# Kernel optimization log

Measured on AMD Instinct MI355X. Metric: run time of the kernel, lower is better.

## Reference

```python
import jax, jax.numpy as jnp
import numpy as np

P = 1024 * 1024  # pixels (coordinate rows) the CPPN is evaluated on
N_IN, H, N_OUT = 12, 32, 3

# Activation library (CPPN-style): 0=identity, 1=tanh, 2=sigmoid, 3=sin, 4=gaussian
_ACTS = [
    lambda x: x,
    jnp.tanh,
    jax.nn.sigmoid,
    jnp.sin,
    lambda x: jnp.exp(-0.5 * x * x),
]

def _apply_acts(pre, ids):
    # pre: [P, n], ids: [n] int per-node activation id (Node.set_activation)
    out = pre
    for k, f in enumerate(_ACTS):
        if k == 0:
            out = f(pre)
        else:
            out = jnp.where(ids == k, f(pre), out)
    return out


def setup_inputs() -> dict:
    key = jax.random.key(0)
    ks = jax.random.split(key, 12)
    def w(k, shape, fan_in):
        return jax.random.normal(k, shape, jnp.float32) / np.sqrt(fan_in)
    inputs = jax.random.normal(ks[0], (P, N_IN), jnp.float32)
    return {
        "inputs": inputs,
        "bias_in": jnp.zeros((N_IN,), jnp.float32),
        "W1": w(ks[1], (N_IN, H), N_IN),
        "b1": 0.1 * jax.random.normal(ks[2], (H,), jnp.float32),
        "act1": jax.random.randint(ks[3], (H,), 0, 5, jnp.int32),
        "W2": w(ks[4], (H, H), H),
        "b2": 0.1 * jax.random.normal(ks[5], (H,), jnp.float32),
        "act2": jax.random.randint(ks[6], (H,), 0, 5, jnp.int32),
        "W3": w(ks[7], (H, H), H),
        "b3": 0.1 * jax.random.normal(ks[8], (H,), jnp.float32),
        "act3": jax.random.randint(ks[9], (H,), 0, 5, jnp.int32),
        "Wout": w(ks[10], (H, N_OUT), H),
        "bout": 0.1 * jax.random.normal(ks[11], (N_OUT,), jnp.float32),
    }


def reference(inputs, bias_in, W1, b1, act1, W2, b2, act2, W3, b3, act3, Wout, bout):
    # Input nodes: Node.forward = identity(x + bias)
    h0 = inputs + bias_in
    # Each hidden layer: per-edge scalar multiply + sum (== matvec since fully
    # connected between consecutive layers), then per-node bias + activation.
    h1 = _apply_acts(h0 @ W1 + b1, act1)
    h2 = _apply_acts(h1 @ W2 + b2, act2)
    h3 = _apply_acts(h2 @ W3 + b3, act3)
    # Output nodes use config.output_activation = tanh
    return jnp.tanh(h3 @ Wout + bout)
```

## Files before the change

kernel.cpp:

```cpp
#include <hip/hip_runtime.h>
#include <hip/hip_bf16.h>


#define BLK 256
#define NT 16

constexpr int NIN = 12, HID = 32, NOUT = 3;

typedef __attribute__((ext_vector_type(8))) short short8v;
typedef __attribute__((ext_vector_type(4))) float f32x4;

__device__ __forceinline__ unsigned short f2bf(float f) {
    unsigned u = __builtin_bit_cast(unsigned, f);
    u += 0x7FFFu + ((u >> 16) & 1u);
    return (unsigned short)(u >> 16);
}

__device__ __forceinline__ float tanh_fast(float x) {
    float e = __expf(2.0f * x);
    return 1.0f - 2.0f * __builtin_amdgcn_rcpf(e + 1.0f);
}

__device__ __forceinline__ float act_apply(float x, int id) {
    float e_in = (id == 1) ? (x + x) : ((id == 4) ? (-0.5f * x * x) : -x);
    float e = __expf(e_in);
    float r = __builtin_amdgcn_rcpf(e + 1.0f);
    float res = x;
    res = (id == 1) ? fmaf(-2.0f, r, 1.0f) : res;
    res = (id == 2) ? r : res;
    res = (id == 3) ? __sinf(x) : res;
    res = (id == 4) ? e : res;
    return res;
}

__global__ void __launch_bounds__(BLK, 4) cppn_mfma(
    const float* __restrict__ xin, const float* __restrict__ bin,
    const float* __restrict__ W1, const float* __restrict__ b1, const int* __restrict__ a1,
    const float* __restrict__ W2, const float* __restrict__ b2, const int* __restrict__ a2,
    const float* __restrict__ W3, const float* __restrict__ b3, const int* __restrict__ a3,
    const float* __restrict__ Wo, const float* __restrict__ bo,
    float* __restrict__ out, int Ppix) {
    const int tid = threadIdx.x;
    const int lane = tid & 63;
    const int wid = tid >> 6;
    const int q = lane >> 4;
    const int l15 = lane & 15;

    short8v w1f[2], w2f[2], w3f[2], wof;
#pragma unroll
    for (int t = 0; t < 2; ++t) {
#pragma unroll
        for (int j = 0; j < 8; ++j) {
            int k1 = 8 * q + j;
            float v1 = (k1 < NIN) ? W1[k1 * HID + 16 * t + l15]
                     : (k1 == NIN ? b1[16 * t + l15] : 0.0f);
            w1f[t][j] = (short)f2bf(v1);
            int k2 = 16 * (j >> 2) + 4 * q + (j & 3);
            w2f[t][j] = (short)f2bf(W2[k2 * HID + 16 * t + l15]);
            w3f[t][j] = (short)f2bf(W3[k2 * HID + 16 * t + l15]);
        }
    }
#pragma unroll
    for (int j = 0; j < 8; ++j) {
        int k2 = 16 * (j >> 2) + 4 * q + (j & 3);
        wof[j] = (l15 < NOUT) ? (short)f2bf(Wo[k2 * NOUT + l15]) : (short)0;
    }

    f32x4 b2f[2], b3f[2], bof;
#pragma unroll
    for (int t = 0; t < 2; ++t) {
#pragma unroll
        for (int r = 0; r < 4; ++r) {
            b2f[t][r] = b2[16 * t + 4 * q + r];
            b3f[t][r] = b3[16 * t + 4 * q + r];
        }
    }
#pragma unroll
    for (int r = 0; r < 4; ++r) bof[r] = (q == 0 && r < NOUT) ? bo[r] : 0.0f;

    int a1v[8], a2v[8], a3v[8];
#pragma unroll
    for (int e = 0; e < 8; ++e) {
        int j = 16 * (e >> 2) + 4 * q + (e & 3);
        a1v[e] = a1[j]; a2v[e] = a2[j]; a3v[e] = a3[j];
    }

    float binv[8];
#pragma unroll
    for (int j = 0; j < 8; ++j) {
        int k = 8 * q + j;
        binv[j] = (k < NIN) ? bin[k] : 0.0f;
    }

    const long long waveIdx = (long long)blockIdx.x * (BLK / 64) + wid;
    const long long px0 = waveIdx * (NT * 16);
    const f32x4 z = {0.0f, 0.0f, 0.0f, 0.0f};

    for (int it = 0; it < NT; ++it) {
        const long long px = px0 + it * 16 + l15;
        const bool ok = (px < Ppix);

        short8v b0f = {0, 0, 0, 0, 0, 0, 0, 0};
        if (q == 0) {
            f32x4 xa = ok ? *reinterpret_cast<const f32x4*>(xin + px * NIN)     : z;
            f32x4 xb = ok ? *reinterpret_cast<const f32x4*>(xin + px * NIN + 4) : z;
#pragma unroll
            for (int j = 0; j < 4; ++j) b0f[j]     = (short)f2bf(xa[j] + binv[j]);
#pragma unroll
            for (int j = 0; j < 4; ++j) b0f[4 + j] = (short)f2bf(xb[j] + binv[4 + j]);
        } else if (q == 1) {
            f32x4 xc = ok ? *reinterpret_cast<const f32x4*>(xin + px * NIN + 8) : z;
#pragma unroll
            for (int j = 0; j < 4; ++j) b0f[j] = (short)f2bf(xc[j] + binv[j]);
            b0f[4] = (short)0x3F80;
        }

        f32x4 p0 = __builtin_amdgcn_mfma_f32_16x16x32_bf16(w1f[0], b0f, z, 0, 0, 0);
        f32x4 p1 = __builtin_amdgcn_mfma_f32_16x16x32_bf16(w1f[1], b0f, z, 0, 0, 0);
        short8v hb;
#pragma unroll
        for (int r = 0; r < 4; ++r) hb[r]     = (short)f2bf(act_apply(p0[r], a1v[r]));
#pragma unroll
        for (int r = 0; r < 4; ++r) hb[4 + r] = (short)f2bf(act_apply(p1[r], a1v[4 + r]));

        p0 = __builtin_amdgcn_mfma_f32_16x16x32_bf16(w2f[0], hb, b2f[0], 0, 0, 0);
        p1 = __builtin_amdgcn_mfma_f32_16x16x32_bf16(w2f[1], hb, b2f[1], 0, 0, 0);
#pragma unroll
        for (int r = 0; r < 4; ++r) hb[r]     = (short)f2bf(act_apply(p0[r], a2v[r]));
#pragma unroll
        for (int r = 0; r < 4; ++r) hb[4 + r] = (short)f2bf(act_apply(p1[r], a2v[4 + r]));

        p0 = __builtin_amdgcn_mfma_f32_16x16x32_bf16(w3f[0], hb, b3f[0], 0, 0, 0);
        p1 = __builtin_amdgcn_mfma_f32_16x16x32_bf16(w3f[1], hb, b3f[1], 0, 0, 0);
#pragma unroll
        for (int r = 0; r < 4; ++r) hb[r]     = (short)f2bf(act_apply(p0[r], a3v[r]));
#pragma unroll
        for (int r = 0; r < 4; ++r) hb[4 + r] = (short)f2bf(act_apply(p1[r], a3v[4 + r]));

        f32x4 o = __builtin_amdgcn_mfma_f32_16x16x32_bf16(wof, hb, bof, 0, 0, 0);
        if (q == 0 && ok) {
            out[px * 3 + 0] = tanh_fast(o[0]);
            out[px * 3 + 1] = tanh_fast(o[1]);
            out[px * 3 + 2] = tanh_fast(o[2]);
        }
    }
}

extern "C" void kernel_launch(void* const* d_in, const int* in_sizes, int n_in,
                              void* d_out, int out_size, void* d_ws, size_t ws_size,
                              hipStream_t stream) {
    (void)n_in; (void)out_size; (void)d_ws; (void)ws_size;
    const float* xin = (const float*)d_in[0];
    const float* bin = (const float*)d_in[1];
    const float* W1  = (const float*)d_in[2];
    const float* b1  = (const float*)d_in[3];
    const int*   a1  = (const int*)  d_in[4];
    const float* W2  = (const float*)d_in[5];
    const float* b2  = (const float*)d_in[6];
    const int*   a2  = (const int*)  d_in[7];
    const float* W3  = (const float*)d_in[8];
    const float* b3  = (const float*)d_in[9];
    const int*   a3  = (const int*)  d_in[10];
    const float* Wo  = (const float*)d_in[11];
    const float* bo  = (const float*)d_in[12];
    float* out = (float*)d_out;

    const int Ppix = in_sizes[0] / NIN;
    const int pxPerBlock = (BLK / 64) * NT * 16;
    const int grid = (Ppix + pxPerBlock - 1) / pxPerBlock;
    hipLaunchKernelGGL(cppn_mfma, dim3(grid), dim3(BLK), 0, stream,
                       xin, bin, W1, b1, a1, W2, b2, a2, W3, b3, a3, Wo, bo,
                       out, Ppix);
}
```

Baseline: 202.2 us.

## Use packed bf16 conversion, bit-packed activation ids, exp2 chain and unguarded main kernel

Replaces the manual bf16 rounding with the v_cvt_pk_bf16_f32 instruction, which converts two floats at once. The per-node activation ids are packed into one 32-bit register per layer, so 24 registers of ids are no longer held. The activation evaluation is rewritten around exp2f with a prescaled input, and the pixel loop is kept rolled. A template GUARD parameter splits the launch into a full-block kernel with no bounds checks and a separate tail kernel, which adds a second launch when the pixel count is not a multiple of the block size.

```diff
diff --git a/kernel.cpp b/kernel.cpp
--- a/kernel.cpp
+++ b/kernel.cpp
@@ -9,6 +9,7 @@
 
 typedef __attribute__((ext_vector_type(8))) short short8v;
 typedef __attribute__((ext_vector_type(4))) float f32x4;
+typedef __attribute__((ext_vector_type(4))) unsigned uint4v;
 
 __device__ __forceinline__ unsigned short f2bf(float f) {
     unsigned u = __builtin_bit_cast(unsigned, f);
@@ -16,30 +17,42 @@
     return (unsigned short)(u >> 16);
 }
 
+__device__ __forceinline__ unsigned cvt_pk(float lo, float hi) {
+    unsigned r;
+    asm("v_cvt_pk_bf16_f32 %0, %1, %2" : "=v"(r) : "v"(lo), "v"(hi));
+    return r;
+}
+
 __device__ __forceinline__ float tanh_fast(float x) {
     float e = __expf(2.0f * x);
     return 1.0f - 2.0f * __builtin_amdgcn_rcpf(e + 1.0f);
 }
 
-__device__ __forceinline__ float act_apply(float x, int id) {
-    float e_in = (id == 1) ? (x + x) : ((id == 4) ? (-0.5f * x * x) : -x);
-    float e = __expf(e_in);
+__device__ __forceinline__ float act_chain(float x, int sid) {
+    const float L = 1.4426950408889634f;
+    const bool is1 = (sid == 1), is2 = (sid == 2), is3 = (sid == 3), is4 = (sid == 4);
+    float u = x * L;
+    float ein = is1 ? (u + u) : -u;
+    float g = (u * -0.5f) * x;
+    ein = is4 ? g : ein;
+    float e = exp2f(ein);
     float r = __builtin_amdgcn_rcpf(e + 1.0f);
-    float res = x;
-    res = (id == 1) ? fmaf(-2.0f, r, 1.0f) : res;
-    res = (id == 2) ? r : res;
-    res = (id == 3) ? __sinf(x) : res;
-    res = (id == 4) ? e : res;
-    return res;
-}
-
+    float y = is1 ? fmaf(-2.0f, r, 1.0f) : x;
+    y = is2 ? r : y;
+    y = is4 ? e : y;
+    float s = __sinf(x);
+    y = is3 ? s : y;
+    return y;
+}
+
+template <bool GUARD>
 __global__ void __launch_bounds__(BLK, 4) cppn_mfma(
     const float* __restrict__ xin, const float* __restrict__ bin,
     const float* __restrict__ W1, const float* __restrict__ b1, const int* __restrict__ a1,
     const float* __restrict__ W2, const float* __restrict__ b2, const int* __restrict__ a2,
     const float* __restrict__ W3, const float* __restrict__ b3, const int* __restrict__ a3,
     const float* __restrict__ Wo, const float* __restrict__ bo,
-    float* __restrict__ out, int Ppix) {
+    float* __restrict__ out, int Ppix, int pxBase) {
     const int tid = threadIdx.x;
     const int lane = tid & 63;
     const int wid = tid >> 6;
@@ -55,35 +68,44 @@
             float v1 = (k1 < NIN) ? W1[k1 * HID + 16 * t + l15]
                      : (k1 == NIN ? b1[16 * t + l15] : 0.0f);
             w1f[t][j] = (short)f2bf(v1);
-            int k2 = 16 * (j >> 2) + 4 * q + (j & 3);
-            w2f[t][j] = (short)f2bf(W2[k2 * HID + 16 * t + l15]);
-            w3f[t][j] = (short)f2bf(W3[k2 * HID + 16 * t + l15]);
+            int kk = 16 * (j >> 2) + 4 * q + (j & 3);
+            w2f[t][j] = (short)f2bf(W2[kk * HID + 16 * t + l15]);
+            w3f[t][j] = (short)f2bf(W3[kk * HID + 16 * t + l15]);
         }
     }
 #pragma unroll
     for (int j = 0; j < 8; ++j) {
-        int k2 = 16 * (j >> 2) + 4 * q + (j & 3);
-        wof[j] = (l15 < NOUT) ? (short)f2bf(Wo[k2 * NOUT + l15]) : (short)0;
+        int kk = 16 * (j >> 2) + 4 * q + (j & 3);
+        wof[j] = (l15 < NOUT) ? (short)f2bf(Wo[kk * NOUT + l15]) : (short)0;
     }
 
     f32x4 b2f[2], b3f[2], bof;
-#pragma unroll
-    for (int t = 0; t < 2; ++t) {
-#pragma unroll
-        for (int r = 0; r < 4; ++r) {
-            b2f[t][r] = b2[16 * t + 4 * q + r];
-            b3f[t][r] = b3[16 * t + 4 * q + r];
-        }
+    unsigned av1 = 0, av2 = 0, av3 = 0;
+#pragma unroll
+    for (int e = 0; e < 8; ++e) {
+        int t = e >> 2, r = e & 3;
+        int idx = 16 * t + 4 * q + r;
+        b2f[t][r] = b2[idx];
+        b3f[t][r] = b3[idx];
+        av1 |= (unsigned)(a1[idx] & 15) << (4 * e);
+        av2 |= (unsigned)(a2[idx] & 15) << (4 * e);
+        av3 |= (unsigned)(a3[idx] & 15) << (4 * e);
     }
 #pragma unroll
     for (int r = 0; r < 4; ++r) bof[r] = (q == 0 && r < NOUT) ? bo[r] : 0.0f;
 
-    int a1v[8], a2v[8], a3v[8];
-#pragma unroll
-    for (int e = 0; e < 8; ++e) {
-        int j = 16 * (e >> 2) + 4 * q + (e & 3);
-        a1v[e] = a1[j]; a2v[e] = a2[j]; a3v[e] = a3[j];
-    }
+    auto actpack = [&](f32x4 p0, f32x4 p1, unsigned av) -> uint4v {
+        float h[8];
+#pragma unroll
+        for (int e = 0; e < 8; ++e) {
+            float x = (e < 4) ? p0[e] : p1[e - 4];
+            h[e] = act_chain(x, (int)((av >> (4 * e)) & 15u));
+        }
+        uint4v w;
+        w[0] = cvt_pk(h[0], h[1]); w[1] = cvt_pk(h[2], h[3]);
+        w[2] = cvt_pk(h[4], h[5]); w[3] = cvt_pk(h[6], h[7]);
+        return w;
+    };
 
     float binv[8];
 #pragma unroll
@@ -92,56 +114,56 @@
         binv[j] = (k < NIN) ? bin[k] : 0.0f;
     }
 
-    const long long waveIdx = (long long)blockIdx.x * (BLK / 64) + wid;
-    const long long px0 = waveIdx * (NT * 16);
+    const long long wIdx = (long long)blockIdx.x * (BLK / 64) + wid;
+    const long long px0 = (long long)pxBase + wIdx * (NT * 16);
+    const float* __restrict__ xbase = xin + px0 * NIN;
+    float* __restrict__ obase = out + px0 * 3;
     const f32x4 z = {0.0f, 0.0f, 0.0f, 0.0f};
 
+#pragma unroll 1
     for (int it = 0; it < NT; ++it) {
-        const long long px = px0 + it * 16 + l15;
-        const bool ok = (px < Ppix);
-
-        short8v b0f = {0, 0, 0, 0, 0, 0, 0, 0};
+        const int po = it * 16 + l15;
+        const bool ok = !GUARD || (px0 + po < (long long)Ppix);
+
+        uint4v b0w = {0, 0, 0, 0};
         if (q == 0) {
-            f32x4 xa = ok ? *reinterpret_cast<const f32x4*>(xin + px * NIN)     : z;
-            f32x4 xb = ok ? *reinterpret_cast<const f32x4*>(xin + px * NIN + 4) : z;
-#pragma unroll
-            for (int j = 0; j < 4; ++j) b0f[j]     = (short)f2bf(xa[j] + binv[j]);
-#pragma unroll
-            for (int j = 0; j < 4; ++j) b0f[4 + j] = (short)f2bf(xb[j] + binv[4 + j]);
+            if (ok) {
+                const float4* ip = reinterpret_cast<const float4*>(xbase + po * NIN);
+                float4 xa = ip[0], xb = ip[1];
+                b0w[0] = cvt_pk(xa.x + binv[0], xa.y + binv[1]);
+                b0w[1] = cvt_pk(xa.z + binv[2], xa.w + binv[3]);
+                b0w[2] = cvt_pk(xb.x + binv[4], xb.y + binv[5]);
+                b0w[3] = cvt_pk(xb.z + binv[6], xb.w + binv[7]);
+            }
         } else if (q == 1) {
-            f32x4 xc = ok ? *reinterpret_cast<const f32x4*>(xin + px * NIN + 8) : z;
-#pragma unroll
-            for (int j = 0; j < 4; ++j) b0f[j] = (short)f2bf(xc[j] + binv[j]);
-            b0f[4] = (short)0x3F80;
-        }
-
-        f32x4 p0 = __builtin_amdgcn_mfma_f32_16x16x32_bf16(w1f[0], b0f, z, 0, 0, 0);
-        f32x4 p1 = __builtin_amdgcn_mfma_f32_16x16x32_bf16(w1f[1], b0f, z, 0, 0, 0);
-        short8v hb;
-#pragma unroll
-        for (int r = 0; r < 4; ++r) hb[r]     = (short)f2bf(act_apply(p0[r], a1v[r]));
-#pragma unroll
-        for (int r = 0; r < 4; ++r) hb[4 + r] = (short)f2bf(act_apply(p1[r], a1v[4 + r]));
-
+            if (ok) {
+                float4 xc = reinterpret_cast<const float4*>(xbase + po * NIN)[2];
+                b0w[0] = cvt_pk(xc.x + binv[0], xc.y + binv[1]);
+                b0w[1] = cvt_pk(xc.z + binv[2], xc.w + binv[3]);
+            }
+            b0w[2] = 0x3F80u;
+        }
+
+        short8v hb = __builtin_bit_cast(short8v, b0w);
+        f32x4 p0 = __builtin_amdgcn_mfma_f32_16x16x32_bf16(w1f[0], hb, z, 0, 0, 0);
+        f32x4 p1 = __builtin_amdgcn_mfma_f32_16x16x32_bf16(w1f[1], hb, z, 0, 0, 0);
+
+        hb = __builtin_bit_cast(short8v, actpack(p0, p1, av1));
         p0 = __builtin_amdgcn_mfma_f32_16x16x32_bf16(w2f[0], hb, b2f[0], 0, 0, 0);
         p1 = __builtin_amdgcn_mfma_f32_16x16x32_bf16(w2f[1], hb, b2f[1], 0, 0, 0);
-#pragma unroll
-        for (int r = 0; r < 4; ++r) hb[r]     = (short)f2bf(act_apply(p0[r], a2v[r]));
-#pragma unroll
-        for (int r = 0; r < 4; ++r) hb[4 + r] = (short)f2bf(act_apply(p1[r], a2v[4 + r]));
-
+
+        hb = __builtin_bit_cast(short8v, actpack(p0, p1, av2));
         p0 = __builtin_amdgcn_mfma_f32_16x16x32_bf16(w3f[0], hb, b3f[0], 0, 0, 0);
         p1 = __builtin_amdgcn_mfma_f32_16x16x32_bf16(w3f[1], hb, b3f[1], 0, 0, 0);
-#pragma unroll
-        for (int r = 0; r < 4; ++r) hb[r]     = (short)f2bf(act_apply(p0[r], a3v[r]));
-#pragma unroll
-        for (int r = 0; r < 4; ++r) hb[4 + r] = (short)f2bf(act_apply(p1[r], a3v[4 + r]));
-
-        f32x4 o = __builtin_amdgcn_mfma_f32_16x16x32_bf16(wof, hb, bof, 0, 0, 0);
+
+        hb = __builtin_bit_cast(short8v, actpack(p0, p1, av3));
+        f32x4 o4 = __builtin_amdgcn_mfma_f32_16x16x32_bf16(wof, hb, bof, 0, 0, 0);
+
         if (q == 0 && ok) {
-            out[px * 3 + 0] = tanh_fast(o[0]);
-            out[px * 3 + 1] = tanh_fast(o[1]);
-            out[px * 3 + 2] = tanh_fast(o[2]);
+            float* op = obase + po * 3;
+            op[0] = tanh_fast(o4[0]);
+            op[1] = tanh_fast(o4[1]);
+            op[2] = tanh_fast(o4[2]);
         }
     }
 }
@@ -167,8 +189,14 @@
 
     const int Ppix = in_sizes[0] / NIN;
     const int pxPerBlock = (BLK / 64) * NT * 16;
-    const int grid = (Ppix + pxPerBlock - 1) / pxPerBlock;
-    hipLaunchKernelGGL(cppn_mfma, dim3(grid), dim3(BLK), 0, stream,
-                       xin, bin, W1, b1, a1, W2, b2, a2, W3, b3, a3, Wo, bo,
-                       out, Ppix);
-}
+    const int fullBlocks = Ppix / pxPerBlock;
+    const int rem = Ppix - fullBlocks * pxPerBlock;
+    if (fullBlocks > 0)
+        hipLaunchKernelGGL((cppn_mfma<false>), dim3(fullBlocks), dim3(BLK), 0, stream,
+                           xin, bin, W1, b1, a1, W2, b2, a2, W3, b3, a3, Wo, bo,
+                           out, Ppix, 0);
+    if (rem > 0)
+        hipLaunchKernelGGL((cppn_mfma<true>), dim3(1), dim3(BLK), 0, stream,
+                           xin, bin, W1, b1, a1, W2, b2, a2, W3, b3, a3, Wo, bo,
+                           out, Ppix, fullBlocks * pxPerBlock);
+}
```

After: 189.5 us. -6.3%, faster.
